# Kernel optimization log

Hardware: AMD Instinct MI355X
Metric: run time of the kernel (lower is better)

Reference implementation:

```python
import jax, jax.numpy as jnp
import numpy as np

N = 50000      # nodes
E = 800000     # graph edges
NNZ = 800000   # hypergraph incidence entries
M = 10000      # hyperedges
IN, HID, OUT = 128, 64, 64


def setup_inputs() -> dict:
    key = jax.random.key(0)
    ks = jax.random.split(key, 12)
    x = jax.random.normal(ks[0], (N, IN), dtype=jnp.float32)
    edge_index = jax.random.randint(ks[1], (2, E), 0, N)
    node_idx = jax.random.randint(ks[2], (NNZ,), 0, N)
    he_idx = jax.random.randint(ks[3], (NNZ,), 0, M)
    hyperedge_index = jnp.stack([node_idx, he_idx])
    w = lambda k, fi, fo: jax.random.normal(k, (fi, fo), jnp.float32) / np.sqrt(fi)
    return {
        "x": x,
        "edge_index": edge_index,
        "hyperedge_index": hyperedge_index,
        "gcn1_w": w(ks[4], IN, HID), "gcn1_b": jnp.zeros((HID,), jnp.float32),
        "gcn2_w": w(ks[5], HID, OUT), "gcn2_b": jnp.zeros((OUT,), jnp.float32),
        "hyper1_w": w(ks[6], IN, HID), "hyper1_b": jnp.zeros((HID,), jnp.float32),
        "hyper2_w": w(ks[7], HID, OUT), "hyper2_b": jnp.zeros((OUT,), jnp.float32),
        "fusion_gate": jnp.zeros((1,), jnp.float32),
    }


def gcn_conv(x, edge_index, w, b):
    # PyG GCNConv: add self-loops, symmetric normalization, then aggregate.
    xw = x @ w
    loops = jnp.arange(N)
    row = jnp.concatenate([edge_index[0], loops])  # source j
    col = jnp.concatenate([edge_index[1], loops])  # target i
    deg = jax.ops.segment_sum(jnp.ones_like(col, dtype=xw.dtype), col, num_segments=N)
    dis = jnp.where(deg > 0, jax.lax.rsqrt(jnp.maximum(deg, 1e-12)), 0.0)
    norm = dis[row] * dis[col]
    out = jax.ops.segment_sum(norm[:, None] * xw[row], col, num_segments=N)
    return out + b


def hyper_conv(x, hyperedge_index, w, b):
    # PyG HypergraphConv (no attention, unit hyperedge weights):
    # out = D^{-1} H B^{-1} H^T (X W) + b
    xw = x @ w
    node_idx, he_idx = hyperedge_index[0], hyperedge_index[1]
    ones = jnp.ones((hyperedge_index.shape[1],), dtype=xw.dtype)
    D = jax.ops.segment_sum(ones, node_idx, num_segments=N)   # node degree
    B = jax.ops.segment_sum(ones, he_idx, num_segments=M)     # hyperedge degree
    Dinv = jnp.where(D > 0, 1.0 / jnp.maximum(D, 1e-12), 0.0)
    Binv = jnp.where(B > 0, 1.0 / jnp.maximum(B, 1e-12), 0.0)
    edge_feat = Binv[:, None] * jax.ops.segment_sum(xw[node_idx], he_idx, num_segments=M)
    out = Dinv[:, None] * jax.ops.segment_sum(edge_feat[he_idx], node_idx, num_segments=N)
    return out + b


def reference(x, edge_index, hyperedge_index,
              gcn1_w, gcn1_b, gcn2_w, gcn2_b,
              hyper1_w, hyper1_b, hyper2_w, hyper2_b,
              fusion_gate):
    # dropout is identity in eval mode (deterministic reference)
    x_s = gcn_conv(x, edge_index, gcn1_w, gcn1_b)
    x_s = jax.nn.elu(x_s)
    x_s = gcn_conv(x_s, edge_index, gcn2_w, gcn2_b)
    x_d = hyper_conv(x, hyperedge_index, hyper1_w, hyper1_b)
    x_d = jax.nn.elu(x_d)
    x_d = hyper_conv(x_d, hyperedge_index, hyper2_w, hyper2_b)
    alpha = jax.nn.sigmoid(fusion_gate)  # shape (1,), broadcasts
    z = alpha * x_s + (1.0 - alpha) * x_d
    return (z, x_s, x_d)
```

## Files before the change

kernel.cpp:

```cpp
#include <hip/hip_runtime.h>
#include <hip/hip_bf16.h>

#define N_NODES 50000
#define N_EDGES 800000
#define NNZ_H   800000
#define M_HE    10000
#define F_IN    128
#define F_HID   64

#define SH_E 7
#define NB_E ((N_NODES + 127) >> 7)
#define SH_H 5
#define NB_H ((M_HE + 31) >> 5)
#define SH_N 7
#define NB_N ((N_NODES + 127) >> 7)
#define TILE 4096
#define GB   ((N_EDGES + TILE - 1) / TILE)
#define NBMAX 400
#define KPBMAX 128
#define GG  782
#define GWN 12500

static __device__ __forceinline__ float bf2f(__hip_bfloat16 v) { return __bfloat162float(v); }

__global__ void k_hist_all(const int* __restrict__ e_col, const int* __restrict__ h_idx,
                           const int* __restrict__ n_idx,
                           int* __restrict__ bcntE, int* __restrict__ bcntH, int* __restrict__ bcntN) {
    __shared__ int hE[NB_E], hH[NB_H], hN[NB_N];
    for (int i = threadIdx.x; i < NB_E; i += 256) hE[i] = 0;
    for (int i = threadIdx.x; i < NB_H; i += 256) hH[i] = 0;
    for (int i = threadIdx.x; i < NB_N; i += 256) hN[i] = 0;
    __syncthreads();
    int stride = gridDim.x * 256;
    for (int i = blockIdx.x * 256 + threadIdx.x; i < N_EDGES; i += stride) {
        atomicAdd(&hE[e_col[i] >> SH_E], 1);
        atomicAdd(&hH[h_idx[i] >> SH_H], 1);
        atomicAdd(&hN[n_idx[i] >> SH_N], 1);
    }
    __syncthreads();
    for (int i = threadIdx.x; i < NB_E; i += 256) if (hE[i]) atomicAdd(&bcntE[i], hE[i]);
    for (int i = threadIdx.x; i < NB_H; i += 256) if (hH[i]) atomicAdd(&bcntH[i], hH[i]);
    for (int i = threadIdx.x; i < NB_N; i += 256) if (hN[i]) atomicAdd(&bcntN[i], hN[i]);
}

__device__ void scan_block(const int* __restrict__ in, int* __restrict__ out, int n) {
    __shared__ int s[1024];
    int t = threadIdx.x;
    int chunk = (n + 1023) >> 10;
    int b = t * chunk;
    int e = min(b + chunk, n);
    int sum = 0;
    for (int i = b; i < e; ++i) sum += in[i];
    s[t] = sum;
    __syncthreads();
    for (int d = 1; d < 1024; d <<= 1) {
        int v = (t >= d) ? s[t - d] : 0;
        __syncthreads();
        s[t] += v;
        __syncthreads();
    }
    int run = (t > 0) ? s[t - 1] : 0;
    for (int i = b; i < e; ++i) { int v = in[i]; out[i] = run; run += v; }
}
__global__ void k_scan_buckets(const int* __restrict__ bcntE, int* __restrict__ boffE,
                               const int* __restrict__ bcntH, int* __restrict__ boffH,
                               const int* __restrict__ bcntN, int* __restrict__ boffN) {
    if (blockIdx.x == 0)      scan_block(bcntE, boffE, NB_E);
    else if (blockIdx.x == 1) scan_block(bcntH, boffH, NB_H);
    else                      scan_block(bcntN, boffN, NB_N);
}

__device__ void chunk_scatter(const int* __restrict__ keys, const int* __restrict__ vals,
                              int n, int sh, int nb,
                              const int* __restrict__ boff, int* __restrict__ bcur,
                              int* __restrict__ bk, int blk) {
    __shared__ int h[NBMAX], loc[NBMAX], base[NBMAX], hc[NBMAX];
    __shared__ int buf[TILE];
    __shared__ unsigned short bkt[TILE];
    int t0 = blk * TILE;
    int tend = min(t0 + TILE, n);
    int cnt = tend - t0;
    for (int b = threadIdx.x; b < nb; b += 256) { h[b] = 0; hc[b] = 0; }
    __syncthreads();
    for (int i = t0 + threadIdx.x; i < tend; i += 256)
        atomicAdd(&h[keys[i] >> sh], 1);
    __syncthreads();
    if (threadIdx.x == 0) {
        int run = 0;
        for (int b = 0; b < nb; ++b) { loc[b] = run; run += h[b]; }
    }
    __syncthreads();
    for (int b = threadIdx.x; b < nb; b += 256)
        base[b] = boff[b] + atomicAdd(&bcur[b], h[b]);
    __syncthreads();
    for (int i = t0 + threadIdx.x; i < tend; i += 256) {
        int k = keys[i];
        int b = k >> sh;
        int r = loc[b] + atomicAdd(&hc[b], 1);
        buf[r] = ((k - (b << sh)) << 16) | vals[i];
        bkt[r] = (unsigned short)b;
    }
    __syncthreads();
    for (int j = threadIdx.x; j < cnt; j += 256) {
        int b = bkt[j];
        bk[base[b] + (j - loc[b])] = buf[j];
    }
}
__global__ void k_chunk_all(const int* __restrict__ e_row, const int* __restrict__ e_col,
                            const int* __restrict__ n_idx, const int* __restrict__ h_idx,
                            const int* __restrict__ boffE, int* __restrict__ bcurE, int* __restrict__ bkE,
                            const int* __restrict__ boffH, int* __restrict__ bcurH, int* __restrict__ bkH,
                            const int* __restrict__ boffN, int* __restrict__ bcurN, int* __restrict__ bkN) {
    int gb = blockIdx.x;
    if (gb < GB)            chunk_scatter(e_col, e_row, N_EDGES, SH_E, NB_E, boffE, bcurE, bkE, gb);
    else if (gb < 2 * GB)   chunk_scatter(h_idx, n_idx, NNZ_H,  SH_H, NB_H, boffH, bcurH, bkH, gb - GB);
    else                    chunk_scatter(n_idx, h_idx, NNZ_H,  SH_N, NB_N, boffN, bcurN, bkN, gb - 2 * GB);
}

__global__ void k_fin_all(const int* __restrict__ bkE, const int* __restrict__ boffE,
                          int* __restrict__ srtE, int* __restrict__ offE,
                          const int* __restrict__ bkH, const int* __restrict__ boffH,
                          int* __restrict__ srtH, int* __restrict__ offH,
                          const int* __restrict__ bkN, const int* __restrict__ boffN,
                          int* __restrict__ srtN, int* __restrict__ offN) {
    __shared__ int koff[KPBMAX];
    __shared__ int kcur[KPBMAX];
    __shared__ int tsum[256];
    int b = blockIdx.x;
    const int* bk; const int* boff; int* srt; int* off;
    int nb, sh, nkeys, total;
    if (b < NB_E) {
        bk = bkE; boff = boffE; srt = srtE; off = offE;
        nb = NB_E; sh = SH_E; nkeys = N_NODES; total = N_EDGES;
    } else if (b < NB_E + NB_H) {
        b -= NB_E;
        bk = bkH; boff = boffH; srt = srtH; off = offH;
        nb = NB_H; sh = SH_H; nkeys = M_HE; total = NNZ_H;
    } else {
        b -= NB_E + NB_H;
        bk = bkN; boff = boffN; srt = srtN; off = offN;
        nb = NB_N; sh = SH_N; nkeys = N_NODES; total = NNZ_H;
    }
    int kpb = 1 << sh;
    int k0 = b << sh;
    int beg = boff[b];
    int end = (b + 1 < nb) ? boff[b + 1] : total;
    int t = threadIdx.x;
    if (t < kpb) { koff[t] = 0; kcur[t] = 0; }
    __syncthreads();
    for (int i = beg + t; i < end; i += 256)
        atomicAdd(&koff[((unsigned)bk[i]) >> 16], 1);
    __syncthreads();
    int v = (t < kpb) ? koff[t] : 0;
    tsum[t] = v;
    __syncthreads();
    for (int d = 1; d < 256; d <<= 1) {
        int u = (t >= d) ? tsum[t - d] : 0;
        __syncthreads();
        tsum[t] += u;
        __syncthreads();
    }
    if (t < kpb) koff[t] = tsum[t] - v;
    __syncthreads();
    if (t < kpb && (k0 + t) < nkeys) off[k0 + t] = beg + koff[t];
    if (b == nb - 1 && t == 0) off[nkeys] = total;
    for (int i = beg + t; i < end; i += 256) {
        int p = bk[i];
        int lk = ((unsigned)p) >> 16;
        int pos = beg + koff[lk] + atomicAdd(&kcur[lk], 1);
        srt[pos] = p & 0xFFFF;
    }
}

template<int K, bool SCALE>
__global__ void k_gemm(const float* __restrict__ xin, const float* __restrict__ w,
                       const int* __restrict__ offE, __hip_bfloat16* __restrict__ out) {
    __shared__ float wl[64 * 64];
    __shared__ float xs[64 * 68];
    int tid = threadIdx.x;
    int wv = tid >> 6, lane = tid & 63;
    int cg = lane & 15;
    int rg = lane >> 4;
    int rl = wv * 16 + rg * 4;
    int r0 = blockIdx.x * 64;
    float acc[4][4] = {};
    for (int k0 = 0; k0 < K; k0 += 64) {
        {
            const float4* wsrc = (const float4*)(w + k0 * 64);
            float4* wdst = (float4*)wl;
            for (int j = tid; j < 1024; j += 256) wdst[j] = wsrc[j];
        }
        for (int p = tid; p < 1024; p += 256) {
            int r = p >> 4, c4 = p & 15;
            int row = min(r0 + r, N_NODES - 1);
            float4 vv = *(const float4*)(xin + (size_t)row * K + k0 + 4 * c4);
            *(float4*)&xs[r * 68 + 4 * c4] = vv;
        }
        __syncthreads();
#pragma unroll 4
        for (int kk = 0; kk < 64; ++kk) {
            float4 wf = *(const float4*)&wl[kk * 64 + cg * 4];
            float x0 = xs[(rl + 0) * 68 + kk];
            float x1 = xs[(rl + 1) * 68 + kk];
            float x2 = xs[(rl + 2) * 68 + kk];
            float x3 = xs[(rl + 3) * 68 + kk];
            acc[0][0] += x0 * wf.x; acc[0][1] += x0 * wf.y; acc[0][2] += x0 * wf.z; acc[0][3] += x0 * wf.w;
            acc[1][0] += x1 * wf.x; acc[1][1] += x1 * wf.y; acc[1][2] += x1 * wf.z; acc[1][3] += x1 * wf.w;
            acc[2][0] += x2 * wf.x; acc[2][1] += x2 * wf.y; acc[2][2] += x2 * wf.z; acc[2][3] += x2 * wf.w;
            acc[3][0] += x3 * wf.x; acc[3][1] += x3 * wf.y; acc[3][2] += x3 * wf.z; acc[3][3] += x3 * wf.w;
        }
        __syncthreads();
    }
#pragma unroll
    for (int i = 0; i < 4; ++i) {
        int row = r0 + rl + i;
        if (row < N_NODES) {
            float s = 1.0f;
            if (SCALE) {
                float deg = (float)(offE[row + 1] - offE[row]);
                s = rsqrtf(deg + 1.0f);
            }
            __hip_bfloat16 hv[4];
            hv[0] = __float2bfloat16(acc[i][0] * s);
            hv[1] = __float2bfloat16(acc[i][1] * s);
            hv[2] = __float2bfloat16(acc[i][2] * s);
            hv[3] = __float2bfloat16(acc[i][3] * s);
            *(ushort4*)&out[(size_t)row * 64 + cg * 4] = *(ushort4*)hv;
        }
    }
}

template<bool ELU>
__global__ __launch_bounds__(256, 8)
void k_gcn_gather(const int* __restrict__ off, const int* __restrict__ srcs,
                  const __hip_bfloat16* __restrict__ xw, const float* __restrict__ b,
                  float* __restrict__ out) {
    int wid = (blockIdx.x * blockDim.x + threadIdx.x) >> 6;
    int f = threadIdx.x & 63;
    if (wid >= N_NODES) return;
    int beg = off[wid], end = off[wid + 1];
    float a0 = 0, a1 = 0, a2 = 0, a3 = 0, a4 = 0, a5 = 0, a6 = 0, a7 = 0;
    int e = beg;
    for (; e + 8 <= end; e += 8) {
        int s0 = srcs[e], s1 = srcs[e + 1], s2 = srcs[e + 2], s3 = srcs[e + 3];
        int s4 = srcs[e + 4], s5 = srcs[e + 5], s6 = srcs[e + 6], s7 = srcs[e + 7];
        a0 += bf2f(xw[(size_t)s0 * 64 + f]);
        a1 += bf2f(xw[(size_t)s1 * 64 + f]);
        a2 += bf2f(xw[(size_t)s2 * 64 + f]);
        a3 += bf2f(xw[(size_t)s3 * 64 + f]);
        a4 += bf2f(xw[(size_t)s4 * 64 + f]);
        a5 += bf2f(xw[(size_t)s5 * 64 + f]);
        a6 += bf2f(xw[(size_t)s6 * 64 + f]);
        a7 += bf2f(xw[(size_t)s7 * 64 + f]);
    }
    for (; e < end; ++e) a0 += bf2f(xw[(size_t)srcs[e] * 64 + f]);
    float acc = ((a0 + a1) + (a2 + a3)) + ((a4 + a5) + (a6 + a7));
    float di = rsqrtf((float)(end - beg) + 1.0f);
    float v = di * (acc + bf2f(xw[(size_t)wid * 64 + f])) + b[f];
    if (ELU) v = (v > 0.0f) ? v : expm1f(v);
    out[(size_t)wid * 64 + f] = v;
}

__global__ __launch_bounds__(256, 8)
void k_he_gather(const int* __restrict__ off, const int* __restrict__ nodes,
                 const __hip_bfloat16* __restrict__ xw, float* __restrict__ C) {
    __shared__ float red[4][64];
    int he = blockIdx.x;
    int wv = threadIdx.x >> 6, f = threadIdx.x & 63;
    int beg = off[he], end = off[he + 1];
    int cnt = end - beg;
    int per = (cnt + 3) >> 2;
    int b0 = beg + wv * per;
    int e0 = min(b0 + per, end);
    float a0 = 0, a1 = 0, a2 = 0, a3 = 0;
    int e = b0;
    for (; e + 4 <= e0; e += 4) {
        int s0 = nodes[e], s1 = nodes[e + 1], s2 = nodes[e + 2], s3 = nodes[e + 3];
        a0 += bf2f(xw[(size_t)s0 * 64 + f]);
        a1 += bf2f(xw[(size_t)s1 * 64 + f]);
        a2 += bf2f(xw[(size_t)s2 * 64 + f]);
        a3 += bf2f(xw[(size_t)s3 * 64 + f]);
    }
    for (; e < e0; ++e) a0 += bf2f(xw[(size_t)nodes[e] * 64 + f]);
    red[wv][f] = (a0 + a1) + (a2 + a3);
    __syncthreads();
    if (wv == 0) {
        float tot = (red[0][f] + red[1][f]) + (red[2][f] + red[3][f]);
        float binv = (cnt > 0) ? 1.0f / (float)cnt : 0.0f;
        C[(size_t)he * 64 + f] = binv * tot;
    }
}

template<bool ELU, bool FUSE>
__global__ __launch_bounds__(256, 8)
void k_node_gather(const int* __restrict__ off, const int* __restrict__ hes,
                   const float* __restrict__ C, const float* __restrict__ b,
                   float* __restrict__ out,
                   const float* __restrict__ xs, const float* __restrict__ gate,
                   float* __restrict__ z) {
    int wid = (blockIdx.x * blockDim.x + threadIdx.x) >> 6;
    int f = threadIdx.x & 63;
    if (wid >= N_NODES) return;
    int beg = off[wid], end = off[wid + 1];
    float a0 = 0, a1 = 0, a2 = 0, a3 = 0, a4 = 0, a5 = 0, a6 = 0, a7 = 0;
    int e = beg;
    for (; e + 8 <= end; e += 8) {
        int s0 = hes[e], s1 = hes[e + 1], s2 = hes[e + 2], s3 = hes[e + 3];
        int s4 = hes[e + 4], s5 = hes[e + 5], s6 = hes[e + 6], s7 = hes[e + 7];
        a0 += C[(size_t)s0 * 64 + f];
        a1 += C[(size_t)s1 * 64 + f];
        a2 += C[(size_t)s2 * 64 + f];
        a3 += C[(size_t)s3 * 64 + f];
        a4 += C[(size_t)s4 * 64 + f];
        a5 += C[(size_t)s5 * 64 + f];
        a6 += C[(size_t)s6 * 64 + f];
        a7 += C[(size_t)s7 * 64 + f];
    }
    for (; e < end; ++e) a0 += C[(size_t)hes[e] * 64 + f];
    float acc = ((a0 + a1) + (a2 + a3)) + ((a4 + a5) + (a6 + a7));
    float dinv = (end > beg) ? 1.0f / (float)(end - beg) : 0.0f;
    float v = dinv * acc + b[f];
    if (ELU) v = (v > 0.0f) ? v : expm1f(v);
    size_t idx = (size_t)wid * 64 + f;
    out[idx] = v;
    if (FUSE) {
        float a = 1.0f / (1.0f + expf(-gate[0]));
        z[idx] = a * xs[idx] + (1.0f - a) * v;
    }
}

extern "C" void kernel_launch(void* const* d_in, const int* in_sizes, int n_in,
                              void* d_out, int out_size, void* d_ws, size_t ws_size,
                              hipStream_t stream) {
    const float* x      = (const float*)d_in[0];
    const int*   ei     = (const int*)d_in[1];
    const int*   hei    = (const int*)d_in[2];
    const float* gcn1_w = (const float*)d_in[3];
    const float* gcn1_b = (const float*)d_in[4];
    const float* gcn2_w = (const float*)d_in[5];
    const float* gcn2_b = (const float*)d_in[6];
    const float* hyp1_w = (const float*)d_in[7];
    const float* hyp1_b = (const float*)d_in[8];
    const float* hyp2_w = (const float*)d_in[9];
    const float* hyp2_b = (const float*)d_in[10];
    const float* gate   = (const float*)d_in[11];
    float* out = (float*)d_out;

    const int* e_row = ei;
    const int* e_col = ei + N_EDGES;
    const int* n_idx = hei;
    const int* h_idx = hei + NNZ_H;

    const size_t NV = (size_t)N_NODES * 64;
    float* z_out  = out;
    float* xs_out = out + NV;
    float* xd_out = out + 2 * NV;

    char* base = (char*)d_ws;
    __hip_bfloat16* Abf = (__hip_bfloat16*)base;
    __hip_bfloat16* Bbf = (__hip_bfloat16*)(base + NV * 2);
    float* AGG1 = (float*)(base + NV * 4);
    float* AGG2 = (float*)(base + NV * 4 + NV * 4);
    float* C    = (float*)(base + NV * 12);
    int* srtE = (int*)(C + (size_t)M_HE * 64);
    int* srtH = srtE + N_EDGES;
    int* srtN = srtH + NNZ_H;
    int* offE = srtN + NNZ_H;
    int* offH = offE + (N_NODES + 1);
    int* offN = offH + (M_HE + 1);
    int* bcntE = offN + (N_NODES + 1);
    int* bcntH = bcntE + NB_E;
    int* bcntN = bcntH + NB_H;
    int* bcurE = bcntN + NB_N;
    int* bcurH = bcurE + NB_E;
    int* bcurN = bcurH + NB_H;
    int* boffE = bcurN + NB_N;
    int* boffH = boffE + NB_E;
    int* boffN = boffH + NB_H;
    const size_t zero_ints = 2 * (size_t)(NB_E + NB_H + NB_N);
    int* bkE = (int*)Abf;
    int* bkH = (int*)Bbf;
    int* bkN = (int*)AGG1;

    const int BLK = 256;

    hipMemsetAsync(bcntE, 0, zero_ints * sizeof(int), stream);
    k_hist_all<<<256, BLK, 0, stream>>>(e_col, h_idx, n_idx, bcntE, bcntH, bcntN);
    k_scan_buckets<<<3, 1024, 0, stream>>>(bcntE, boffE, bcntH, boffH, bcntN, boffN);
    k_chunk_all<<<3 * GB, BLK, 0, stream>>>(e_row, e_col, n_idx, h_idx,
                                            boffE, bcurE, bkE,
                                            boffH, bcurH, bkH,
                                            boffN, bcurN, bkN);
    k_fin_all<<<NB_E + NB_H + NB_N, BLK, 0, stream>>>(bkE, boffE, srtE, offE,
                                                      bkH, boffH, srtH, offH,
                                                      bkN, boffN, srtN, offN);

    k_gemm<F_IN, true><<<GG, BLK, 0, stream>>>(x, gcn1_w, offE, Abf);
    k_gcn_gather<true><<<GWN, BLK, 0, stream>>>(offE, srtE, Abf, gcn1_b, AGG1);

    k_gemm<F_HID, true><<<GG, BLK, 0, stream>>>(AGG1, gcn2_w, offE, Abf);
    k_gcn_gather<false><<<GWN, BLK, 0, stream>>>(offE, srtE, Abf, gcn2_b, xs_out);

    k_gemm<F_IN, false><<<GG, BLK, 0, stream>>>(x, hyp1_w, nullptr, Bbf);
    k_he_gather<<<M_HE, BLK, 0, stream>>>(offH, srtH, Bbf, C);
    k_node_gather<true, false><<<GWN, BLK, 0, stream>>>(offN, srtN, C, hyp1_b, AGG2,
                                                        nullptr, nullptr, nullptr);

    k_gemm<F_HID, false><<<GG, BLK, 0, stream>>>(AGG2, hyp2_w, nullptr, Bbf);
    k_he_gather<<<M_HE, BLK, 0, stream>>>(offH, srtH, Bbf, C);
    k_node_gather<false, true><<<GWN, BLK, 0, stream>>>(offN, srtN, C, hyp2_b, xd_out,
                                                        xs_out, gate, z_out);

    (void)in_sizes; (void)n_in; (void)out_size; (void)ws_size;
}
```

Baseline: 322.6 us.

## Merge GCN and hypergraph branches into dual kernels and vectorize bf16 gathers

The GEMMs of the GCN and hypergraph branches now run together in one launch, and so do the GCN gather and hyperedge gather, by splitting the grid on block index. This cuts the number of kernel launches and lets independent work fill the GPU at the same time. The gather kernels now read packed bf16 pairs as 32-bit words, with two half-waves each handling alternate edges and combining through a cross-lane shuffle. The node gather also reads float2 from C. The trade-off is more divergent code per kernel, plus possible load imbalance between the two halves of each grid.

```diff
diff --git a/kernel.cpp b/kernel.cpp
--- a/kernel.cpp
+++ b/kernel.cpp
@@ -21,7 +21,8 @@
 #define GG  782
 #define GWN 12500
 
-static __device__ __forceinline__ float bf2f(__hip_bfloat16 v) { return __bfloat162float(v); }
+static __device__ __forceinline__ float bflo(unsigned v) { return __uint_as_float(v << 16); }
+static __device__ __forceinline__ float bfhi(unsigned v) { return __uint_as_float(v & 0xFFFF0000u); }
 
 __global__ void k_hist_all(const int* __restrict__ e_col, const int* __restrict__ h_idx,
                            const int* __restrict__ n_idx,
@@ -173,16 +174,15 @@
 }
 
 template<int K, bool SCALE>
-__global__ void k_gemm(const float* __restrict__ xin, const float* __restrict__ w,
-                       const int* __restrict__ offE, __hip_bfloat16* __restrict__ out) {
-    __shared__ float wl[64 * 64];
-    __shared__ float xs[64 * 68];
+__device__ __forceinline__ void gemm_body(const float* __restrict__ xin, const float* __restrict__ w,
+                                          const int* __restrict__ offE, __hip_bfloat16* __restrict__ out,
+                                          int blk, float* __restrict__ wl, float* __restrict__ xs) {
     int tid = threadIdx.x;
     int wv = tid >> 6, lane = tid & 63;
     int cg = lane & 15;
     int rg = lane >> 4;
     int rl = wv * 16 + rg * 4;
-    int r0 = blockIdx.x * 64;
+    int r0 = blk * 64;
     float acc[4][4] = {};
     for (int k0 = 0; k0 < K; k0 += 64) {
         {
@@ -230,65 +230,115 @@
     }
 }
 
+template<int K>
+__global__ void k_gemm_dual(const float* __restrict__ in1, const float* __restrict__ w1,
+                            const int* __restrict__ offE, __hip_bfloat16* __restrict__ out1,
+                            const float* __restrict__ in2, const float* __restrict__ w2,
+                            __hip_bfloat16* __restrict__ out2) {
+    __shared__ float wl[64 * 64];
+    __shared__ float xs[64 * 68];
+    if (blockIdx.x < GG) gemm_body<K, true>(in1, w1, offE, out1, blockIdx.x, wl, xs);
+    else                 gemm_body<K, false>(in2, w2, nullptr, out2, blockIdx.x - GG, wl, xs);
+}
+
 template<bool ELU>
-__global__ __launch_bounds__(256, 8)
-void k_gcn_gather(const int* __restrict__ off, const int* __restrict__ srcs,
-                  const __hip_bfloat16* __restrict__ xw, const float* __restrict__ b,
-                  float* __restrict__ out) {
-    int wid = (blockIdx.x * blockDim.x + threadIdx.x) >> 6;
-    int f = threadIdx.x & 63;
+__device__ __forceinline__ void gcn_gather_body(const int* __restrict__ off, const int* __restrict__ srcs,
+                                                const __hip_bfloat16* __restrict__ xw,
+                                                const float* __restrict__ b,
+                                                float* __restrict__ out, int blk) {
+    int tid = threadIdx.x;
+    int wv = tid >> 6, lane = tid & 63;
+    int h = lane >> 5, l = lane & 31;
+    int wid = blk * 4 + wv;
     if (wid >= N_NODES) return;
-    int beg = off[wid], end = off[wid + 1];
-    float a0 = 0, a1 = 0, a2 = 0, a3 = 0, a4 = 0, a5 = 0, a6 = 0, a7 = 0;
-    int e = beg;
-    for (; e + 8 <= end; e += 8) {
-        int s0 = srcs[e], s1 = srcs[e + 1], s2 = srcs[e + 2], s3 = srcs[e + 3];
-        int s4 = srcs[e + 4], s5 = srcs[e + 5], s6 = srcs[e + 6], s7 = srcs[e + 7];
-        a0 += bf2f(xw[(size_t)s0 * 64 + f]);
-        a1 += bf2f(xw[(size_t)s1 * 64 + f]);
-        a2 += bf2f(xw[(size_t)s2 * 64 + f]);
-        a3 += bf2f(xw[(size_t)s3 * 64 + f]);
-        a4 += bf2f(xw[(size_t)s4 * 64 + f]);
-        a5 += bf2f(xw[(size_t)s5 * 64 + f]);
-        a6 += bf2f(xw[(size_t)s6 * 64 + f]);
-        a7 += bf2f(xw[(size_t)s7 * 64 + f]);
-    }
-    for (; e < end; ++e) a0 += bf2f(xw[(size_t)srcs[e] * 64 + f]);
-    float acc = ((a0 + a1) + (a2 + a3)) + ((a4 + a5) + (a6 + a7));
-    float di = rsqrtf((float)(end - beg) + 1.0f);
-    float v = di * (acc + bf2f(xw[(size_t)wid * 64 + f])) + b[f];
-    if (ELU) v = (v > 0.0f) ? v : expm1f(v);
-    out[(size_t)wid * 64 + f] = v;
-}
-
-__global__ __launch_bounds__(256, 8)
-void k_he_gather(const int* __restrict__ off, const int* __restrict__ nodes,
-                 const __hip_bfloat16* __restrict__ xw, float* __restrict__ C) {
-    __shared__ float red[4][64];
-    int he = blockIdx.x;
-    int wv = threadIdx.x >> 6, f = threadIdx.x & 63;
+    int beg = off[wid];
+    int cnt = off[wid + 1] - beg;
+    const unsigned* xwu = (const unsigned*)xw;
+    float ax0 = 0, ay0 = 0, ax1 = 0, ay1 = 0, ax2 = 0, ay2 = 0, ax3 = 0, ay3 = 0;
+    int k = h;
+    for (; k + 6 < cnt; k += 8) {
+        int s0 = srcs[beg + k];
+        int s1 = srcs[beg + k + 2];
+        int s2 = srcs[beg + k + 4];
+        int s3 = srcs[beg + k + 6];
+        unsigned v0 = xwu[(size_t)s0 * 32 + l];
+        unsigned v1 = xwu[(size_t)s1 * 32 + l];
+        unsigned v2 = xwu[(size_t)s2 * 32 + l];
+        unsigned v3 = xwu[(size_t)s3 * 32 + l];
+        ax0 += bflo(v0); ay0 += bfhi(v0);
+        ax1 += bflo(v1); ay1 += bfhi(v1);
+        ax2 += bflo(v2); ay2 += bfhi(v2);
+        ax3 += bflo(v3); ay3 += bfhi(v3);
+    }
+    for (; k < cnt; k += 2) {
+        unsigned v = xwu[(size_t)srcs[beg + k] * 32 + l];
+        ax0 += bflo(v); ay0 += bfhi(v);
+    }
+    float tx = (ax0 + ax1) + (ax2 + ax3);
+    float ty = (ay0 + ay1) + (ay2 + ay3);
+    tx += __shfl_xor(tx, 32);
+    ty += __shfl_xor(ty, 32);
+    unsigned sv = xwu[(size_t)wid * 32 + l];
+    float di = rsqrtf((float)cnt + 1.0f);
+    float vx = di * (tx + bflo(sv)) + b[2 * l];
+    float vy = di * (ty + bfhi(sv)) + b[2 * l + 1];
+    if (ELU) {
+        vx = (vx > 0.0f) ? vx : expm1f(vx);
+        vy = (vy > 0.0f) ? vy : expm1f(vy);
+    }
+    if (h == 0) *(float2*)(out + (size_t)wid * 64 + 2 * l) = make_float2(vx, vy);
+}
+
+__device__ __forceinline__ void he_gather_body(const int* __restrict__ off, const int* __restrict__ nodes,
+                                               const __hip_bfloat16* __restrict__ xw,
+                                               float* __restrict__ C, int he, float2 (*red)[32]) {
+    int tid = threadIdx.x;
+    int wv = tid >> 6, lane = tid & 63;
+    int h = lane >> 5, l = lane & 31;
     int beg = off[he], end = off[he + 1];
     int cnt = end - beg;
     int per = (cnt + 3) >> 2;
     int b0 = beg + wv * per;
     int e0 = min(b0 + per, end);
-    float a0 = 0, a1 = 0, a2 = 0, a3 = 0;
-    int e = b0;
-    for (; e + 4 <= e0; e += 4) {
-        int s0 = nodes[e], s1 = nodes[e + 1], s2 = nodes[e + 2], s3 = nodes[e + 3];
-        a0 += bf2f(xw[(size_t)s0 * 64 + f]);
-        a1 += bf2f(xw[(size_t)s1 * 64 + f]);
-        a2 += bf2f(xw[(size_t)s2 * 64 + f]);
-        a3 += bf2f(xw[(size_t)s3 * 64 + f]);
-    }
-    for (; e < e0; ++e) a0 += bf2f(xw[(size_t)nodes[e] * 64 + f]);
-    red[wv][f] = (a0 + a1) + (a2 + a3);
-    __syncthreads();
-    if (wv == 0) {
-        float tot = (red[0][f] + red[1][f]) + (red[2][f] + red[3][f]);
+    int c2 = e0 - b0;
+    const unsigned* xwu = (const unsigned*)xw;
+    float ax0 = 0, ay0 = 0, ax1 = 0, ay1 = 0;
+    int k = h;
+    for (; k + 2 < c2; k += 4) {
+        unsigned v0 = xwu[(size_t)nodes[b0 + k] * 32 + l];
+        unsigned v1 = xwu[(size_t)nodes[b0 + k + 2] * 32 + l];
+        ax0 += bflo(v0); ay0 += bfhi(v0);
+        ax1 += bflo(v1); ay1 += bfhi(v1);
+    }
+    for (; k < c2; k += 2) {
+        unsigned v = xwu[(size_t)nodes[b0 + k] * 32 + l];
+        ax0 += bflo(v); ay0 += bfhi(v);
+    }
+    float tx = ax0 + ax1;
+    float ty = ay0 + ay1;
+    tx += __shfl_xor(tx, 32);
+    ty += __shfl_xor(ty, 32);
+    if (h == 0) red[wv][l] = make_float2(tx, ty);
+    __syncthreads();
+    if (tid < 32) {
+        float2 r0 = red[0][tid], r1 = red[1][tid], r2 = red[2][tid], r3 = red[3][tid];
         float binv = (cnt > 0) ? 1.0f / (float)cnt : 0.0f;
-        C[(size_t)he * 64 + f] = binv * tot;
-    }
+        float2 o = make_float2((r0.x + r1.x + r2.x + r3.x) * binv,
+                               (r0.y + r1.y + r2.y + r3.y) * binv);
+        *(float2*)(C + (size_t)he * 64 + 2 * tid) = o;
+    }
+}
+
+template<bool ELU>
+__global__ __launch_bounds__(256, 8)
+void k_gather_dual(const int* __restrict__ offE, const int* __restrict__ srtE,
+                   const __hip_bfloat16* __restrict__ A, const float* __restrict__ gb,
+                   float* __restrict__ aggOut,
+                   const int* __restrict__ offH, const int* __restrict__ srtH,
+                   const __hip_bfloat16* __restrict__ B, float* __restrict__ C) {
+    __shared__ float2 red[4][32];
+    if (blockIdx.x < GWN) gcn_gather_body<ELU>(offE, srtE, A, gb, aggOut, blockIdx.x);
+    else                  he_gather_body(offH, srtH, B, C, blockIdx.x - GWN, red);
 }
 
 template<bool ELU, bool FUSE>
@@ -298,34 +348,49 @@
                    float* __restrict__ out,
                    const float* __restrict__ xs, const float* __restrict__ gate,
                    float* __restrict__ z) {
-    int wid = (blockIdx.x * blockDim.x + threadIdx.x) >> 6;
-    int f = threadIdx.x & 63;
+    int tid = threadIdx.x;
+    int wv = tid >> 6, lane = tid & 63;
+    int h = lane >> 5, l = lane & 31;
+    int wid = blockIdx.x * 4 + wv;
     if (wid >= N_NODES) return;
-    int beg = off[wid], end = off[wid + 1];
-    float a0 = 0, a1 = 0, a2 = 0, a3 = 0, a4 = 0, a5 = 0, a6 = 0, a7 = 0;
-    int e = beg;
-    for (; e + 8 <= end; e += 8) {
-        int s0 = hes[e], s1 = hes[e + 1], s2 = hes[e + 2], s3 = hes[e + 3];
-        int s4 = hes[e + 4], s5 = hes[e + 5], s6 = hes[e + 6], s7 = hes[e + 7];
-        a0 += C[(size_t)s0 * 64 + f];
-        a1 += C[(size_t)s1 * 64 + f];
-        a2 += C[(size_t)s2 * 64 + f];
-        a3 += C[(size_t)s3 * 64 + f];
-        a4 += C[(size_t)s4 * 64 + f];
-        a5 += C[(size_t)s5 * 64 + f];
-        a6 += C[(size_t)s6 * 64 + f];
-        a7 += C[(size_t)s7 * 64 + f];
-    }
-    for (; e < end; ++e) a0 += C[(size_t)hes[e] * 64 + f];
-    float acc = ((a0 + a1) + (a2 + a3)) + ((a4 + a5) + (a6 + a7));
-    float dinv = (end > beg) ? 1.0f / (float)(end - beg) : 0.0f;
-    float v = dinv * acc + b[f];
-    if (ELU) v = (v > 0.0f) ? v : expm1f(v);
-    size_t idx = (size_t)wid * 64 + f;
-    out[idx] = v;
-    if (FUSE) {
-        float a = 1.0f / (1.0f + expf(-gate[0]));
-        z[idx] = a * xs[idx] + (1.0f - a) * v;
+    int beg = off[wid];
+    int cnt = off[wid + 1] - beg;
+    float ax0 = 0, ay0 = 0, ax1 = 0, ay1 = 0, ax2 = 0, ay2 = 0, ax3 = 0, ay3 = 0;
+    int k = h;
+    for (; k + 6 < cnt; k += 8) {
+        float2 c0 = *(const float2*)(C + (size_t)hes[beg + k] * 64 + 2 * l);
+        float2 c1 = *(const float2*)(C + (size_t)hes[beg + k + 2] * 64 + 2 * l);
+        float2 c2 = *(const float2*)(C + (size_t)hes[beg + k + 4] * 64 + 2 * l);
+        float2 c3 = *(const float2*)(C + (size_t)hes[beg + k + 6] * 64 + 2 * l);
+        ax0 += c0.x; ay0 += c0.y;
+        ax1 += c1.x; ay1 += c1.y;
+        ax2 += c2.x; ay2 += c2.y;
+        ax3 += c3.x; ay3 += c3.y;
+    }
+    for (; k < cnt; k += 2) {
+        float2 c = *(const float2*)(C + (size_t)hes[beg + k] * 64 + 2 * l);
+        ax0 += c.x; ay0 += c.y;
+    }
+    float tx = (ax0 + ax1) + (ax2 + ax3);
+    float ty = (ay0 + ay1) + (ay2 + ay3);
+    tx += __shfl_xor(tx, 32);
+    ty += __shfl_xor(ty, 32);
+    float dinv = (cnt > 0) ? 1.0f / (float)cnt : 0.0f;
+    float vx = dinv * tx + b[2 * l];
+    float vy = dinv * ty + b[2 * l + 1];
+    if (ELU) {
+        vx = (vx > 0.0f) ? vx : expm1f(vx);
+        vy = (vy > 0.0f) ? vy : expm1f(vy);
+    }
+    if (h == 0) {
+        size_t idx = (size_t)wid * 64 + 2 * l;
+        *(float2*)(out + idx) = make_float2(vx, vy);
+        if (FUSE) {
+            float a = 1.0f / (1.0f + expf(-gate[0]));
+            float2 s = *(const float2*)(xs + idx);
+            *(float2*)(z + idx) = make_float2(a * s.x + (1.0f - a) * vx,
+                                              a * s.y + (1.0f - a) * vy);
+        }
     }
 }
 
@@ -360,7 +425,7 @@
     __hip_bfloat16* Abf = (__hip_bfloat16*)base;
     __hip_bfloat16* Bbf = (__hip_bfloat16*)(base + NV * 2);
     float* AGG1 = (float*)(base + NV * 4);
-    float* AGG2 = (float*)(base + NV * 4 + NV * 4);
+    float* AGG2 = (float*)(base + NV * 8);
     float* C    = (float*)(base + NV * 12);
     int* srtE = (int*)(C + (size_t)M_HE * 64);
     int* srtH = srtE + N_EDGES;
@@ -395,19 +460,14 @@
                                                       bkH, boffH, srtH, offH,
                                                       bkN, boffN, srtN, offN);
 
-    k_gemm<F_IN, true><<<GG, BLK, 0, stream>>>(x, gcn1_w, offE, Abf);
-    k_gcn_gather<true><<<GWN, BLK, 0, stream>>>(offE, srtE, Abf, gcn1_b, AGG1);
-
-    k_gemm<F_HID, true><<<GG, BLK, 0, stream>>>(AGG1, gcn2_w, offE, Abf);
-    k_gcn_gather<false><<<GWN, BLK, 0, stream>>>(offE, srtE, Abf, gcn2_b, xs_out);
-
-    k_gemm<F_IN, false><<<GG, BLK, 0, stream>>>(x, hyp1_w, nullptr, Bbf);
-    k_he_gather<<<M_HE, BLK, 0, stream>>>(offH, srtH, Bbf, C);
+    k_gemm_dual<F_IN><<<2 * GG, BLK, 0, stream>>>(x, gcn1_w, offE, Abf, x, hyp1_w, Bbf);
+    k_gather_dual<true><<<GWN + M_HE, BLK, 0, stream>>>(offE, srtE, Abf, gcn1_b, AGG1,
+                                                        offH, srtH, Bbf, C);
     k_node_gather<true, false><<<GWN, BLK, 0, stream>>>(offN, srtN, C, hyp1_b, AGG2,
                                                         nullptr, nullptr, nullptr);
-
-    k_gemm<F_HID, false><<<GG, BLK, 0, stream>>>(AGG2, hyp2_w, nullptr, Bbf);
-    k_he_gather<<<M_HE, BLK, 0, stream>>>(offH, srtH, Bbf, C);
+    k_gemm_dual<F_HID><<<2 * GG, BLK, 0, stream>>>(AGG1, gcn2_w, offE, Abf, AGG2, hyp2_w, Bbf);
+    k_gather_dual<false><<<GWN + M_HE, BLK, 0, stream>>>(offE, srtE, Abf, gcn2_b, xs_out,
+                                                         offH, srtH, Bbf, C);
     k_node_gather<false, true><<<GWN, BLK, 0, stream>>>(offN, srtN, C, hyp2_b, xd_out,
                                                         xs_out, gate, z_out);
 
```

New measurement: 279.8 us. 1.15x faster.
